# Optimization experiments

Hardware: AMD Instinct MI355X
Metric: run time of the kernel (lower is better)

## Reference

```python
import jax, jax.numpy as jnp
import numpy as np

D = 512
H = 8
HD = D // H
EPS = 1e-6


def layer_norm(x, a, b):
    # torch: std is unbiased (ddof=1); note division by (std + eps), not sqrt(var+eps)
    mean = x.mean(-1, keepdims=True)
    std = jnp.sqrt(x.var(-1, ddof=1, keepdims=True))
    return a * (x - mean) / (std + EPS) + b


def setup_inputs() -> dict:
    key = jax.random.key(0)
    ks = jax.random.split(key, 8)
    x = jax.random.normal(ks[0], (4, 2048, D), dtype=jnp.float32)
    s = 0.02
    return {
        "x": x,
        "ln1_a": jnp.ones((D,), jnp.float32),
        "ln1_b": jnp.zeros((D,), jnp.float32),
        "ln2_a": jnp.ones((D,), jnp.float32),
        "ln2_b": jnp.zeros((D,), jnp.float32),
        "wq": jax.random.normal(ks[1], (D, D), jnp.float32) * s,  # [out, in] torch layout
        "wk": jax.random.normal(ks[2], (D, D), jnp.float32) * s,
        "wv": jax.random.normal(ks[3], (D, D), jnp.float32) * s,
        "wo": jax.random.normal(ks[4], (D, D), jnp.float32) * s,
        "w1": jax.random.normal(ks[5], (D, D), jnp.float32) * s,  # MLP hidden == dim
        "b1": jnp.zeros((D,), jnp.float32),
        "w2": jax.random.normal(ks[6], (D, D), jnp.float32) * s,
        "b2": jnp.zeros((D,), jnp.float32),
    }


def reference(x, ln1_a, ln1_b, ln2_a, ln2_b, wq, wk, wv, wo, w1, b1, w2, b2):
    B, S, _ = x.shape
    xn = layer_norm(x, ln1_a, ln1_b)
    # attention (non-causal, dropout=identity in eval)
    q = (xn @ wq.T).reshape(B, S, H, HD)
    k = (xn @ wk.T).reshape(B, S, H, HD)
    v = (xn @ wv.T).reshape(B, S, H, HD)
    scores = jnp.einsum("bshd,bthd->bhst", q, k) / jnp.sqrt(jnp.float32(HD))
    probs = jax.nn.softmax(scores.astype(jnp.float32), axis=-1).astype(q.dtype)
    attn = jnp.einsum("bhst,bthd->bshd", probs, v).reshape(B, S, D)
    h = xn + attn @ wo.T
    # MLP
    hn = layer_norm(h, ln2_a, ln2_b)
    ffn = jax.nn.relu(hn @ w1.T + b1) @ w2.T + b2
    return h + ffn
```

## Files before the change

kernel.cpp:

```cpp
#include <hip/hip_runtime.h>


typedef short s16x8 __attribute__((ext_vector_type(8)));
typedef float f32x4 __attribute__((ext_vector_type(4)));
typedef unsigned short u16;
typedef u16 u16x4 __attribute__((ext_vector_type(4)));

__device__ __forceinline__ u16 f2b(float f) {
  union { float f; unsigned u; } c; c.f = f;
  return (u16)((c.u + 0x7FFFu + ((c.u >> 16) & 1u)) >> 16);
}

__device__ __forceinline__ f32x4 mfma16(s16x8 a, s16x8 b, f32x4 c) {
  return __builtin_amdgcn_mfma_f32_16x16x32_bf16(a, b, c, 0, 0, 0);
}

__device__ __forceinline__ void gload_lds16(const u16* g, u16* l) {
  __builtin_amdgcn_global_load_lds(
      (const __attribute__((address_space(1))) unsigned*)g,
      (__attribute__((address_space(3))) unsigned*)l, 16, 0, 0);
}

__global__ __launch_bounds__(256) void cast_w(
    const float* __restrict__ s0, const float* __restrict__ s1,
    const float* __restrict__ s2, const float* __restrict__ s3,
    const float* __restrict__ s4, const float* __restrict__ s5,
    u16* __restrict__ dst)
{
  int i = blockIdx.x * 256 + threadIdx.x;
  const float* s;
  switch (blockIdx.y) {
    case 0: s = s0; break; case 1: s = s1; break; case 2: s = s2; break;
    case 3: s = s3; break; case 4: s = s4; break; default: s = s5; break;
  }
  float4 v = ((const float4*)s)[i];
  u16x4 o; o.x = f2b(v.x); o.y = f2b(v.y); o.z = f2b(v.z); o.w = f2b(v.w);
  *(u16x4*)(dst + (size_t)blockIdx.y * 262144 + (size_t)i * 4) = o;
}

template<int OF, int OB>
__global__ __launch_bounds__(256) void ln_kernel(
    const float* __restrict__ x, const float* __restrict__ ga,
    const float* __restrict__ gbv, float* __restrict__ yf, u16* __restrict__ yb)
{
  int row = blockIdx.x * 4 + (threadIdx.x >> 6);
  int lane = threadIdx.x & 63;
  size_t base = (size_t)row * 512 + lane * 8;
  const float4* xr = (const float4*)(x + base);
  float4 v0 = xr[0], v1 = xr[1];
  float s  = v0.x + v0.y + v0.z + v0.w + v1.x + v1.y + v1.z + v1.w;
  float ss = v0.x*v0.x + v0.y*v0.y + v0.z*v0.z + v0.w*v0.w
           + v1.x*v1.x + v1.y*v1.y + v1.z*v1.z + v1.w*v1.w;
  #pragma unroll
  for (int m = 1; m < 64; m <<= 1) { s += __shfl_xor(s, m); ss += __shfl_xor(ss, m); }
  float mean = s * (1.0f / 512.0f);
  float var  = fmaxf((ss - 512.0f * mean * mean) * (1.0f / 511.0f), 0.0f);
  float inv  = 1.0f / (sqrtf(var) + 1e-6f);
  const float4* ap = (const float4*)(ga + lane * 8);
  const float4* bp = (const float4*)(gbv + lane * 8);
  float4 a0 = ap[0], a1 = ap[1], b0 = bp[0], b1 = bp[1];
  float4 y0, y1;
  y0.x = (v0.x-mean)*inv*a0.x + b0.x;  y0.y = (v0.y-mean)*inv*a0.y + b0.y;
  y0.z = (v0.z-mean)*inv*a0.z + b0.z;  y0.w = (v0.w-mean)*inv*a0.w + b0.w;
  y1.x = (v1.x-mean)*inv*a1.x + b1.x;  y1.y = (v1.y-mean)*inv*a1.y + b1.y;
  y1.z = (v1.z-mean)*inv*a1.z + b1.z;  y1.w = (v1.w-mean)*inv*a1.w + b1.w;
  if (OF) { float4* o = (float4*)(yf + base); o[0] = y0; o[1] = y1; }
  if (OB) {
    union { s16x8 v; u16 u[8]; } pk;
    pk.u[0]=f2b(y0.x); pk.u[1]=f2b(y0.y); pk.u[2]=f2b(y0.z); pk.u[3]=f2b(y0.w);
    pk.u[4]=f2b(y1.x); pk.u[5]=f2b(y1.y); pk.u[6]=f2b(y1.z); pk.u[7]=f2b(y1.w);
    *(s16x8*)(yb + base) = pk.v;
  }
}

template<int MODE>
__global__ __launch_bounds__(256) void gemm128(
    const u16* __restrict__ A, const u16* __restrict__ W,
    const float* __restrict__ bias, const float* __restrict__ resid,
    float* __restrict__ outf, u16* __restrict__ outb,
    u16* __restrict__ outb3, float qscale)
{
  __shared__ u16 als[2][128 * 64];
  __shared__ u16 bls[2][128 * 64];
  int t = threadIdx.x, lane = t & 63, w = t >> 6;
  int l15 = lane & 15, g = lane >> 4;
  int wr = w >> 1, wc = w & 1;
  int mbase = blockIdx.x * 128, nbase = blockIdx.y * 128;

  size_t offA[4], offB[4];
  #pragma unroll
  for (int j = 0; j < 4; ++j) {
    int cid = j * 256 + t;
    int row = cid >> 3, cs = (cid & 7) ^ (row & 7);
    offA[j] = (size_t)(mbase + row) * 512 + cs * 8;
    offB[j] = (size_t)(nbase + row) * 512 + cs * 8;
  }

  #define GSTAGE(buf, k0) do {                                        \
    _Pragma("unroll")                                                 \
    for (int j = 0; j < 4; ++j)                                       \
      gload_lds16(A + (k0) + offA[j], &als[buf][(j * 256 + w * 64) * 8]); \
    _Pragma("unroll")                                                 \
    for (int j = 0; j < 4; ++j)                                       \
      gload_lds16(W + (k0) + offB[j], &bls[buf][(j * 256 + w * 64) * 8]); \
  } while (0)

  int ar[4][2], br[4][2];
  #pragma unroll
  for (int i = 0; i < 4; ++i) {
    int rA = wr * 64 + i * 16 + l15;
    int rB = wc * 64 + i * 16 + l15;
    #pragma unroll
    for (int kh = 0; kh < 2; ++kh) {
      ar[i][kh] = rA * 64 + (((kh * 4 + g) ^ (rA & 7)) << 3);
      br[i][kh] = rB * 64 + (((kh * 4 + g) ^ (rB & 7)) << 3);
    }
  }

  f32x4 zero = {0.0f, 0.0f, 0.0f, 0.0f};
  f32x4 acc[4][4];
  #pragma unroll
  for (int mi = 0; mi < 4; ++mi)
    #pragma unroll
    for (int ni = 0; ni < 4; ++ni) acc[mi][ni] = zero;

  GSTAGE(0, 0);
  __syncthreads();
  int cur = 0;
  for (int kk = 0; kk < 8; ++kk) {
    if (kk < 7) GSTAGE(cur ^ 1, (kk + 1) * 64);
    s16x8 af[4][2], bfr[4][2];
    #pragma unroll
    for (int i = 0; i < 4; ++i) {
      #pragma unroll
      for (int kh = 0; kh < 2; ++kh) {
        af[i][kh]  = *(const s16x8*)&als[cur][ar[i][kh]];
        bfr[i][kh] = *(const s16x8*)&bls[cur][br[i][kh]];
      }
    }
    #pragma unroll
    for (int kh = 0; kh < 2; ++kh)
      #pragma unroll
      for (int mi = 0; mi < 4; ++mi)
        #pragma unroll
        for (int ni = 0; ni < 4; ++ni)
          acc[mi][ni] = mfma16(af[mi][kh], bfr[ni][kh], acc[mi][ni]);
    __syncthreads();
    cur ^= 1;
  }
  #undef GSTAGE

  if (MODE & 128) {
    int bidx = mbase >> 11;
    int Wbase = ((mbase & 2047) >> 5) + wr * 2;
    #pragma unroll
    for (int ni = 0; ni < 4; ++ni) {
      int nn = nbase + wc * 64 + ni * 16 + l15;
      #pragma unroll
      for (int p = 0; p < 2; ++p) {
        union { s16x8 v; u16 u[8]; } pkv;
        #pragma unroll
        for (int r = 0; r < 4; ++r) {
          pkv.u[2 * r]     = f2b(acc[2 * p][ni][r]);
          pkv.u[2 * r + 1] = f2b(acc[2 * p + 1][ni][r]);
        }
        *(s16x8*)(outb3 + ((size_t)((bidx * 64 + Wbase + p) * 512 + nn)) * 32
                  + 8 * g) = pkv.v;
      }
    }
  } else {
    #pragma unroll
    for (int ni = 0; ni < 4; ++ni) {
      int n = nbase + wc * 64 + ni * 16 + l15;
      float bv = (MODE & 1) ? bias[n] : 0.0f;
      #pragma unroll
      for (int mi = 0; mi < 4; ++mi) {
        #pragma unroll
        for (int r = 0; r < 4; ++r) {
          int m = mbase + wr * 64 + mi * 16 + 4 * g + r;
          float v = acc[mi][ni][r] + bv;
          if (MODE & 2) v = fmaxf(v, 0.0f);
          if (MODE & 4) v += resid[(size_t)m * 512 + n];
          if (MODE & 8) outf[(size_t)m * 512 + n] = v;
          if (MODE & 16) {
            float vs = (MODE & 32) ? v * qscale : v;
            outb[(size_t)m * 512 + n] = f2b(vs);
          }
        }
      }
    }
  }
}

__global__ __launch_bounds__(256) void attn_kernel(
    const u16* __restrict__ q, const u16* __restrict__ k,
    const u16* __restrict__ vt, u16* __restrict__ o)
{
  __shared__ u16 kls[4][64 * 64];
  __shared__ u16 vls[4][64 * 64];
  int t = threadIdx.x, lane = t & 63, w = t >> 6;
  int l15 = lane & 15, g = lane >> 4;
  int sw = l15 & 7;
  int lrow = lane >> 3;
  int lchunk = (lane & 7) ^ (lrow & 7);
  int fid = blockIdx.x + 32 * blockIdx.y;
  int xcd = fid & 7, rest = fid >> 3;
  int bh = xcd * 4 + (rest & 3);
  int qt = rest >> 2;
  int bb = bh >> 3, h = bh & 7;
  int qbase = qt * 128 + w * 32;

  const u16* qp = q + (size_t)(bb * 2048 + qbase + l15) * 512 + h * 64 + g * 8;
  s16x8 qf0a = *(const s16x8*)qp;
  s16x8 qf1a = *(const s16x8*)(qp + 32);
  s16x8 qf0b = *(const s16x8*)(qp + 16 * 512);
  s16x8 qf1b = *(const s16x8*)(qp + 16 * 512 + 32);
  f32x4 zero = {0.0f, 0.0f, 0.0f, 0.0f};
  f32x4 oacc[2][4];
  #pragma unroll
  for (int qg = 0; qg < 2; ++qg)
    #pragma unroll
    for (int nf = 0; nf < 4; ++nf) oacc[qg][nf] = zero;
  float lsum[2] = {0.0f, 0.0f};
  const u16* kb0 = k + (size_t)(bb * 2048) * 512 + h * 64;
  const u16* vtw = vt + (size_t)bb * 1048576 + h * 2048;

  #define STAGE(nb, tt) do {                                                  \
    int sr0 = w * 16 + lrow;                                                  \
    const u16* ks0 = kb0 + (size_t)((tt) * 64 + sr0) * 512 + lchunk * 8;      \
    const u16* vs0 = vtw + (size_t)(2 * (tt) + (lchunk >> 2)) * 16384         \
                   + (size_t)sr0 * 32 + (lchunk & 3) * 8;                     \
    gload_lds16(ks0, &kls[nb][(w * 16) * 64]);                                \
    gload_lds16(ks0 + (size_t)8 * 512, &kls[nb][(w * 16 + 8) * 64]);          \
    gload_lds16(vs0, &vls[nb][(w * 16) * 64]);                                \
    gload_lds16(vs0 + 256, &vls[nb][(w * 16 + 8) * 64]);                      \
  } while (0)

  #define QKT(kbuf, sdst) do {                                                \
    _Pragma("unroll")                                                         \
    for (int kg = 0; kg < 4; ++kg) {                                          \
      int rb = (kg * 16 + l15) * 64;                                          \
      s16x8 ka = *(const s16x8*)&(kbuf)[rb + ((g ^ sw) << 3)];                \
      s16x8 kc = *(const s16x8*)&(kbuf)[rb + (((4 + g) ^ sw) << 3)];          \
      sdst[0][kg] = mfma16(ka, qf0a, zero);                                   \
      sdst[0][kg] = mfma16(kc, qf1a, sdst[0][kg]);                            \
      sdst[1][kg] = mfma16(ka, qf0b, zero);                                   \
      sdst[1][kg] = mfma16(kc, qf1b, sdst[1][kg]);                            \
    }                                                                         \
  } while (0)

  #define SMAX(ssrc) do {                                                     \
    _Pragma("unroll")                                                         \
    for (int qg = 0; qg < 2; ++qg) {                                          \
      _Pragma("unroll")                                                       \
      for (int b2 = 0; b2 < 2; ++b2) {                                        \
        _Pragma("unroll")                                                     \
        for (int r = 0; r < 4; ++r) {                                         \
          float p0 = __builtin_amdgcn_exp2f(ssrc[qg][2 * b2][r]);             \
          float p1 = __builtin_amdgcn_exp2f(ssrc[qg][2 * b2 + 1][r]);         \
          lsum[qg] += p0 + p1;                                                \
          union { float f; unsigned u; } ua, ub;                              \
          ua.f = p0; ub.f = p1;                                               \
          pk[qg][b2].u32v[r] = __builtin_amdgcn_perm(ub.u, ua.u, 0x07060302u);\
        }                                                                     \
      }                                                                       \
    }                                                                         \
  } while (0)

  #define PVC(vbuf) do {                                                      \
    _Pragma("unroll")                                                         \
    for (int b2 = 0; b2 < 2; ++b2) {                                          \
      _Pragma("unroll")                                                       \
      for (int nf = 0; nf < 4; ++nf) {                                        \
        s16x8 vf = *(const s16x8*)                                            \
            &(vbuf)[(nf * 16 + l15) * 64 + ((((b2 << 2) | g) ^ sw) << 3)];    \
        oacc[0][nf] = mfma16(pk[0][b2].v8, vf, oacc[0][nf]);                  \
        oacc[1][nf] = mfma16(pk[1][b2].v8, vf, oacc[1][nf]);                  \
      }                                                                       \
    }                                                                         \
  } while (0)

  typedef union { s16x8 v8; unsigned u32v[4]; } pku;

  #define ITER(kt, scur, snxt) do {                                           \
    if ((kt) < 30) asm volatile("s_waitcnt vmcnt(4)" ::: "memory");           \
    else           asm volatile("s_waitcnt vmcnt(0)" ::: "memory");           \
    __builtin_amdgcn_s_barrier();                                             \
    if ((kt) + 3 < 32) STAGE(((kt) + 3) & 3, (kt) + 3);                       \
    if ((kt) + 1 < 32) QKT(kls[((kt) + 1) & 3], snxt);                        \
    pku pk[2][2];                                                             \
    SMAX(scur);                                                               \
    PVC(vls[(kt) & 3]);                                                       \
  } while (0)

  STAGE(0, 0);
  STAGE(1, 1);
  STAGE(2, 2);
  asm volatile("s_waitcnt vmcnt(8)" ::: "memory");
  __builtin_amdgcn_s_barrier();
  f32x4 sA[2][4], sB[2][4];
  QKT(kls[0], sA);

  for (int k2 = 0; k2 < 32; k2 += 2) {
    ITER(k2, sA, sB);
    ITER(k2 + 1, sB, sA);
  }
  #undef ITER
  #undef PVC
  #undef SMAX
  #undef QKT
  #undef STAGE

  #pragma unroll
  for (int qg = 0; qg < 2; ++qg) {
    float ls = lsum[qg];
    ls += __shfl_xor(ls, 16);
    ls += __shfl_xor(ls, 32);
    float linv = 1.0f / ls;
    size_t obase = (size_t)(bb * 2048 + qbase + qg * 16 + 4 * g) * 512
                 + h * 64 + l15;
    #pragma unroll
    for (int r = 0; r < 4; ++r) {
      float lr = __shfl(linv, 4 * g + r);
      #pragma unroll
      for (int nf = 0; nf < 4; ++nf)
        o[obase + (size_t)r * 512 + nf * 16] = f2b(oacc[qg][nf][r] * lr);
    }
  }
}

extern "C" void kernel_launch(void* const* d_in, const int* in_sizes, int n_in,
                              void* d_out, int out_size, void* d_ws, size_t ws_size,
                              hipStream_t stream)
{
  const float* x     = (const float*)d_in[0];
  const float* ln1_a = (const float*)d_in[1];
  const float* ln1_b = (const float*)d_in[2];
  const float* ln2_a = (const float*)d_in[3];
  const float* ln2_b = (const float*)d_in[4];
  const float* wq = (const float*)d_in[5];
  const float* wk = (const float*)d_in[6];
  const float* wv = (const float*)d_in[7];
  const float* wo = (const float*)d_in[8];
  const float* w1 = (const float*)d_in[9];
  const float* b1 = (const float*)d_in[10];
  const float* w2 = (const float*)d_in[11];
  const float* b2 = (const float*)d_in[12];

  char* ws = (char*)d_ws;
  float* xn_f = (float*)(ws + (size_t)0);
  float* h_f  = (float*)(ws + ((size_t)16 << 20));
  u16* xn_b = (u16*)(ws + ((size_t)32 << 20));
  u16* q_b  = (u16*)(ws + ((size_t)40 << 20));
  u16* k_b  = (u16*)(ws + ((size_t)48 << 20));
  u16* vt_b = (u16*)(ws + ((size_t)56 << 20));
  u16* at_b = (u16*)(ws + ((size_t)64 << 20));
  u16* wb   = (u16*)(ws + ((size_t)72 << 20));
  u16 *wkb = wb + 262144, *wvb = wb + 2 * 262144;
  u16 *wob = wb + 3 * 262144, *w1b = wb + 4 * 262144, *w2b = wb + 5 * 262144;
  u16* hn_b = q_b;
  u16* f_b  = at_b;

  dim3 blk(256);
  dim3 g512(64, 4);
  cast_w<<<dim3(256, 6), blk, 0, stream>>>(wq, wk, wv, wo, w1, w2, wb);
  ln_kernel<1, 1><<<dim3(2048), blk, 0, stream>>>(x, ln1_a, ln1_b, xn_f, xn_b);
  gemm128<128><<<g512, blk, 0, stream>>>(
      xn_b, wvb, nullptr, nullptr, nullptr, nullptr, vt_b, 0.0f);
  gemm128<16><<<g512, blk, 0, stream>>>(
      xn_b, wkb, nullptr, nullptr, nullptr, k_b, nullptr, 0.0f);
  gemm128<16 | 32><<<g512, blk, 0, stream>>>(
      xn_b, wb, nullptr, nullptr, nullptr, q_b, nullptr, 0.18033688f);
  attn_kernel<<<dim3(32, 16), blk, 0, stream>>>(q_b, k_b, vt_b, at_b);
  gemm128<4 | 8><<<g512, blk, 0, stream>>>(
      at_b, wob, nullptr, xn_f, h_f, nullptr, nullptr, 0.0f);
  ln_kernel<0, 1><<<dim3(2048), blk, 0, stream>>>(h_f, ln2_a, ln2_b, nullptr, hn_b);
  gemm128<1 | 2 | 16><<<g512, blk, 0, stream>>>(
      hn_b, w1b, b1, nullptr, nullptr, f_b, nullptr, 0.0f);
  gemm128<1 | 4 | 8><<<g512, blk, 0, stream>>>(
      f_b, w2b, b2, h_f, (float*)d_out, nullptr, nullptr, 0.0f);
}
```

Before: 130.3 us.

## Restructure attention pipeline to process two KV tiles per barrier phase

Reworks the attention K/V software pipeline so each barrier phase stages two tiles and processes two tiles, with a 6-deep V LDS ring and 4-deep K ring. This halves the number of block barriers and waitcnt points per KV sweep. The cost is more LDS (extra V buffers), more live score registers (four score sets instead of two), and a full vmcnt(0) wait each phase instead of a partial one, which may reduce load/compute overlap and occupancy.

```diff
diff --git a/kernel.cpp b/kernel.cpp
--- a/kernel.cpp
+++ b/kernel.cpp
@@ -197,7 +197,7 @@
     const u16* __restrict__ vt, u16* __restrict__ o)
 {
   __shared__ u16 kls[4][64 * 64];
-  __shared__ u16 vls[4][64 * 64];
+  __shared__ u16 vls[6][64 * 64];
   int t = threadIdx.x, lane = t & 63, w = t >> 6;
   int l15 = lane & 15, g = lane >> 4;
   int sw = l15 & 7;
@@ -225,15 +225,17 @@
   const u16* kb0 = k + (size_t)(bb * 2048) * 512 + h * 64;
   const u16* vtw = vt + (size_t)bb * 1048576 + h * 2048;
 
-  #define STAGE(nb, tt) do {                                                  \
+  #define STAGE(tt) do {                                                      \
     int sr0 = w * 16 + lrow;                                                  \
     const u16* ks0 = kb0 + (size_t)((tt) * 64 + sr0) * 512 + lchunk * 8;      \
     const u16* vs0 = vtw + (size_t)(2 * (tt) + (lchunk >> 2)) * 16384         \
                    + (size_t)sr0 * 32 + (lchunk & 3) * 8;                     \
-    gload_lds16(ks0, &kls[nb][(w * 16) * 64]);                                \
-    gload_lds16(ks0 + (size_t)8 * 512, &kls[nb][(w * 16 + 8) * 64]);          \
-    gload_lds16(vs0, &vls[nb][(w * 16) * 64]);                                \
-    gload_lds16(vs0 + 256, &vls[nb][(w * 16 + 8) * 64]);                      \
+    u16* kd = &kls[(tt) & 3][0];                                              \
+    u16* vd = &vls[(tt) % 6][0];                                              \
+    gload_lds16(ks0, kd + (w * 16) * 64);                                     \
+    gload_lds16(ks0 + (size_t)8 * 512, kd + (w * 16 + 8) * 64);               \
+    gload_lds16(vs0, vd + (w * 16) * 64);                                     \
+    gload_lds16(vs0 + 256, vd + (w * 16 + 8) * 64);                           \
   } while (0)
 
   #define QKT(kbuf, sdst) do {                                                \
@@ -282,30 +284,61 @@
 
   typedef union { s16x8 v8; unsigned u32v[4]; } pku;
 
-  #define ITER(kt, scur, snxt) do {                                           \
-    if ((kt) < 30) asm volatile("s_waitcnt vmcnt(4)" ::: "memory");           \
-    else           asm volatile("s_waitcnt vmcnt(0)" ::: "memory");           \
+  #define PHASE(j, c0, c1, n0, n1) do {                                       \
+    asm volatile("s_waitcnt vmcnt(0)" ::: "memory");                          \
     __builtin_amdgcn_s_barrier();                                             \
-    if ((kt) + 3 < 32) STAGE(((kt) + 3) & 3, (kt) + 3);                       \
-    if ((kt) + 1 < 32) QKT(kls[((kt) + 1) & 3], snxt);                        \
-    pku pk[2][2];                                                             \
-    SMAX(scur);                                                               \
-    PVC(vls[(kt) & 3]);                                                       \
-  } while (0)
-
-  STAGE(0, 0);
-  STAGE(1, 1);
-  STAGE(2, 2);
-  asm volatile("s_waitcnt vmcnt(8)" ::: "memory");
+    STAGE(2 * (j) + 4);                                                       \
+    STAGE(2 * (j) + 5);                                                       \
+    {                                                                         \
+      pku pk[2][2];                                                           \
+      QKT(kls[(2 * (j) + 2) & 3], n0);                                        \
+      SMAX(c0);                                                               \
+      PVC(vls[(2 * (j)) % 6]);                                                \
+    }                                                                         \
+    {                                                                         \
+      pku pk[2][2];                                                           \
+      QKT(kls[(2 * (j) + 3) & 3], n1);                                        \
+      SMAX(c1);                                                               \
+      PVC(vls[(2 * (j) + 1) % 6]);                                            \
+    }                                                                         \
+  } while (0)
+
+  STAGE(0); STAGE(1); STAGE(2); STAGE(3);
+  asm volatile("s_waitcnt vmcnt(0)" ::: "memory");
   __builtin_amdgcn_s_barrier();
-  f32x4 sA[2][4], sB[2][4];
-  QKT(kls[0], sA);
-
-  for (int k2 = 0; k2 < 32; k2 += 2) {
-    ITER(k2, sA, sB);
-    ITER(k2 + 1, sB, sA);
-  }
-  #undef ITER
+  f32x4 sA0[2][4], sA1[2][4], sB0[2][4], sB1[2][4];
+  QKT(kls[0], sA0);
+  QKT(kls[1], sA1);
+
+  for (int j = 0; j < 14; j += 2) {
+    PHASE(j,     sA0, sA1, sB0, sB1);
+    PHASE(j + 1, sB0, sB1, sA0, sA1);
+  }
+  asm volatile("s_waitcnt vmcnt(0)" ::: "memory");
+  __builtin_amdgcn_s_barrier();
+  {
+    pku pk[2][2];
+    QKT(kls[30 & 3], sB0);
+    SMAX(sA0);
+    PVC(vls[28 % 6]);
+  }
+  {
+    pku pk[2][2];
+    QKT(kls[31 & 3], sB1);
+    SMAX(sA1);
+    PVC(vls[29 % 6]);
+  }
+  {
+    pku pk[2][2];
+    SMAX(sB0);
+    PVC(vls[30 % 6]);
+  }
+  {
+    pku pk[2][2];
+    SMAX(sB1);
+    PVC(vls[31 % 6]);
+  }
+  #undef PHASE
   #undef PVC
   #undef SMAX
   #undef QKT
```

New measurement: 142.6 us. 1.09x slower.

## Split attention over two key halves and merge partial outputs in a separate kernel

Applied to the files above, without the earlier changes.

The attention grid is doubled so that each block processes only half of the key sequence. Each half writes an unnormalized partial output (fp32 for the first half, bf16 for the second) plus per-row partial sums into spare workspace. A new merge kernel adds the two partials and normalizes them into the bf16 attention output. This is meant to give more blocks per CU and better latency hiding. In exchange it adds an extra kernel launch and a full read/write pass over the partials, and it shrinks the LDS pipeline depth with a full vmcnt(0) wait on every iteration.

```diff
diff --git a/kernel.cpp b/kernel.cpp
--- a/kernel.cpp
+++ b/kernel.cpp
@@ -9,6 +9,11 @@
 __device__ __forceinline__ u16 f2b(float f) {
   union { float f; unsigned u; } c; c.f = f;
   return (u16)((c.u + 0x7FFFu + ((c.u >> 16) & 1u)) >> 16);
+}
+
+__device__ __forceinline__ float b2f(u16 b) {
+  union { unsigned u; float f; } c; c.u = ((unsigned)b) << 16;
+  return c.f;
 }
 
 __device__ __forceinline__ f32x4 mfma16(s16x8 a, s16x8 b, f32x4 c) {
@@ -194,10 +199,11 @@
 
 __global__ __launch_bounds__(256) void attn_kernel(
     const u16* __restrict__ q, const u16* __restrict__ k,
-    const u16* __restrict__ vt, u16* __restrict__ o)
-{
-  __shared__ u16 kls[4][64 * 64];
-  __shared__ u16 vls[4][64 * 64];
+    const u16* __restrict__ vt, float* __restrict__ p0,
+    u16* __restrict__ p1, float* __restrict__ lw)
+{
+  __shared__ u16 kls[2][64 * 64];
+  __shared__ u16 vls[3][64 * 64];
   int t = threadIdx.x, lane = t & 63, w = t >> 6;
   int l15 = lane & 15, g = lane >> 4;
   int sw = l15 & 7;
@@ -206,7 +212,9 @@
   int fid = blockIdx.x + 32 * blockIdx.y;
   int xcd = fid & 7, rest = fid >> 3;
   int bh = xcd * 4 + (rest & 3);
-  int qt = rest >> 2;
+  int qh = rest >> 2;
+  int half = qh & 1, qt = qh >> 1;
+  int T0 = half << 4;
   int bb = bh >> 3, h = bh & 7;
   int qbase = qt * 128 + w * 32;
 
@@ -225,15 +233,18 @@
   const u16* kb0 = k + (size_t)(bb * 2048) * 512 + h * 64;
   const u16* vtw = vt + (size_t)bb * 1048576 + h * 2048;
 
-  #define STAGE(nb, tt) do {                                                  \
+  #define STAGE(ktl) do {                                                     \
+    int tt = T0 + (ktl);                                                      \
     int sr0 = w * 16 + lrow;                                                  \
-    const u16* ks0 = kb0 + (size_t)((tt) * 64 + sr0) * 512 + lchunk * 8;      \
-    const u16* vs0 = vtw + (size_t)(2 * (tt) + (lchunk >> 2)) * 16384         \
+    const u16* ks0 = kb0 + (size_t)(tt * 64 + sr0) * 512 + lchunk * 8;        \
+    const u16* vs0 = vtw + (size_t)(2 * tt + (lchunk >> 2)) * 16384           \
                    + (size_t)sr0 * 32 + (lchunk & 3) * 8;                     \
-    gload_lds16(ks0, &kls[nb][(w * 16) * 64]);                                \
-    gload_lds16(ks0 + (size_t)8 * 512, &kls[nb][(w * 16 + 8) * 64]);          \
-    gload_lds16(vs0, &vls[nb][(w * 16) * 64]);                                \
-    gload_lds16(vs0 + 256, &vls[nb][(w * 16 + 8) * 64]);                      \
+    u16* kd = &kls[(ktl) & 1][0];                                             \
+    u16* vd = &vls[(ktl) % 3][0];                                             \
+    gload_lds16(ks0, kd + (w * 16) * 64);                                     \
+    gload_lds16(ks0 + (size_t)8 * 512, kd + (w * 16 + 8) * 64);               \
+    gload_lds16(vs0, vd + (w * 16) * 64);                                     \
+    gload_lds16(vs0 + 256, vd + (w * 16 + 8) * 64);                           \
   } while (0)
 
   #define QKT(kbuf, sdst) do {                                                \
@@ -256,11 +267,11 @@
       for (int b2 = 0; b2 < 2; ++b2) {                                        \
         _Pragma("unroll")                                                     \
         for (int r = 0; r < 4; ++r) {                                         \
-          float p0 = __builtin_amdgcn_exp2f(ssrc[qg][2 * b2][r]);             \
-          float p1 = __builtin_amdgcn_exp2f(ssrc[qg][2 * b2 + 1][r]);         \
-          lsum[qg] += p0 + p1;                                                \
+          float pp0 = __builtin_amdgcn_exp2f(ssrc[qg][2 * b2][r]);            \
+          float pp1 = __builtin_amdgcn_exp2f(ssrc[qg][2 * b2 + 1][r]);        \
+          lsum[qg] += pp0 + pp1;                                              \
           union { float f; unsigned u; } ua, ub;                              \
-          ua.f = p0; ub.f = p1;                                               \
+          ua.f = pp0; ub.f = pp1;                                             \
           pk[qg][b2].u32v[r] = __builtin_amdgcn_perm(ub.u, ua.u, 0x07060302u);\
         }                                                                     \
       }                                                                       \
@@ -283,25 +294,23 @@
   typedef union { s16x8 v8; unsigned u32v[4]; } pku;
 
   #define ITER(kt, scur, snxt) do {                                           \
-    if ((kt) < 30) asm volatile("s_waitcnt vmcnt(4)" ::: "memory");           \
-    else           asm volatile("s_waitcnt vmcnt(0)" ::: "memory");           \
+    asm volatile("s_waitcnt vmcnt(0)" ::: "memory");                          \
     __builtin_amdgcn_s_barrier();                                             \
-    if ((kt) + 3 < 32) STAGE(((kt) + 3) & 3, (kt) + 3);                       \
-    if ((kt) + 1 < 32) QKT(kls[((kt) + 1) & 3], snxt);                        \
+    if ((kt) + 2 < 16) STAGE((kt) + 2);                                       \
+    if ((kt) + 1 < 16) QKT(kls[((kt) + 1) & 1], snxt);                        \
     pku pk[2][2];                                                             \
     SMAX(scur);                                                               \
-    PVC(vls[(kt) & 3]);                                                       \
-  } while (0)
-
-  STAGE(0, 0);
-  STAGE(1, 1);
-  STAGE(2, 2);
-  asm volatile("s_waitcnt vmcnt(8)" ::: "memory");
+    PVC(vls[(kt) % 3]);                                                       \
+  } while (0)
+
+  STAGE(0);
+  STAGE(1);
+  asm volatile("s_waitcnt vmcnt(4)" ::: "memory");
   __builtin_amdgcn_s_barrier();
   f32x4 sA[2][4], sB[2][4];
   QKT(kls[0], sA);
 
-  for (int k2 = 0; k2 < 32; k2 += 2) {
+  for (int k2 = 0; k2 < 16; k2 += 2) {
     ITER(k2, sA, sB);
     ITER(k2 + 1, sB, sA);
   }
@@ -316,17 +325,46 @@
     float ls = lsum[qg];
     ls += __shfl_xor(ls, 16);
     ls += __shfl_xor(ls, 32);
-    float linv = 1.0f / ls;
+    if (g == 0)
+      lw[half * 65536 + bh * 2048 + qbase + qg * 16 + l15] = ls;
     size_t obase = (size_t)(bb * 2048 + qbase + qg * 16 + 4 * g) * 512
                  + h * 64 + l15;
     #pragma unroll
     for (int r = 0; r < 4; ++r) {
-      float lr = __shfl(linv, 4 * g + r);
       #pragma unroll
-      for (int nf = 0; nf < 4; ++nf)
-        o[obase + (size_t)r * 512 + nf * 16] = f2b(oacc[qg][nf][r] * lr);
+      for (int nf = 0; nf < 4; ++nf) {
+        if (half == 0)
+          p0[obase + (size_t)r * 512 + nf * 16] = oacc[qg][nf][r];
+        else
+          p1[obase + (size_t)r * 512 + nf * 16] = f2b(oacc[qg][nf][r]);
+      }
     }
   }
+}
+
+__global__ __launch_bounds__(256) void merge_o(
+    const float* __restrict__ p0, const u16* __restrict__ p1,
+    const float* __restrict__ lw, u16* __restrict__ o)
+{
+  int row = blockIdx.x * 4 + (threadIdx.x >> 6);
+  int lane = threadIdx.x & 63;
+  int h = lane >> 3;
+  int bh = (row >> 11) * 8 + h;
+  int sidx = row & 2047;
+  float l = lw[bh * 2048 + sidx] + lw[65536 + bh * 2048 + sidx];
+  float inv = 1.0f / l;
+  size_t base = (size_t)row * 512 + lane * 8;
+  f32x4 a0 = ((const f32x4*)(p0 + base))[0];
+  f32x4 a1 = ((const f32x4*)(p0 + base))[1];
+  union { s16x8 v; u16 u[8]; } b;
+  b.v = *(const s16x8*)(p1 + base);
+  union { s16x8 v; u16 u[8]; } out;
+  #pragma unroll
+  for (int j = 0; j < 4; ++j) {
+    out.u[j]     = f2b((a0[j] + b2f(b.u[j]))     * inv);
+    out.u[j + 4] = f2b((a1[j] + b2f(b.u[j + 4])) * inv);
+  }
+  *(s16x8*)(o + base) = out.v;
 }
 
 extern "C" void kernel_launch(void* const* d_in, const int* in_sizes, int n_in,
@@ -358,6 +396,7 @@
   u16* wb   = (u16*)(ws + ((size_t)72 << 20));
   u16 *wkb = wb + 262144, *wvb = wb + 2 * 262144;
   u16 *wob = wb + 3 * 262144, *w1b = wb + 4 * 262144, *w2b = wb + 5 * 262144;
+  float* lw = (float*)wb;
   u16* hn_b = q_b;
   u16* f_b  = at_b;
 
@@ -371,7 +410,8 @@
       xn_b, wkb, nullptr, nullptr, nullptr, k_b, nullptr, 0.0f);
   gemm128<16 | 32><<<g512, blk, 0, stream>>>(
       xn_b, wb, nullptr, nullptr, nullptr, q_b, nullptr, 0.18033688f);
-  attn_kernel<<<dim3(32, 16), blk, 0, stream>>>(q_b, k_b, vt_b, at_b);
+  attn_kernel<<<dim3(32, 32), blk, 0, stream>>>(q_b, k_b, vt_b, h_f, xn_b, lw);
+  merge_o<<<dim3(2048), blk, 0, stream>>>(h_f, xn_b, lw, at_b);
   gemm128<4 | 8><<<g512, blk, 0, stream>>>(
       at_b, wob, nullptr, xn_f, h_f, nullptr, nullptr, 0.0f);
   ln_kernel<0, 1><<<dim3(2048), blk, 0, stream>>>(h_f, ln2_a, ln2_b, nullptr, hn_b);
```

Measured after the change: 137.4 us. 1.05x slower.
